# Kernel tuning notes

Hardware: AMD Instinct MI355X
Metric: run time of the kernel (lower is better)

Reference implementation:

```python
import jax, jax.numpy as jnp
import numpy as np

LN_EPS = 1e-5

def _layernorm(x, w, b):
    mu = jnp.mean(x, axis=-1, keepdims=True)
    var = jnp.mean(jnp.square(x - mu), axis=-1, keepdims=True)
    return (x - mu) * jax.lax.rsqrt(var + LN_EPS) * w + b

def setup_inputs() -> dict:
    key = jax.random.key(0)
    ks = jax.random.split(key, 8)
    B, T, D, E = 8, 4096, 1024, 4
    inner = 4 * D
    x = jax.random.normal(ks[0], (B, T, D), dtype=jnp.float32)
    router_prob = jax.random.uniform(ks[1], (B, T, E), dtype=jnp.float32)
    alpha = jnp.ones((), dtype=jnp.float32)
    norm_w = jnp.ones((D,), dtype=jnp.float32)
    norm_b = jnp.zeros((D,), dtype=jnp.float32)
    l1_w = jax.random.normal(ks[2], (inner, D), dtype=jnp.float32) * 0.02
    l1_b = jax.random.normal(ks[3], (inner,), dtype=jnp.float32) * 0.02
    l2_w = jax.random.normal(ks[4], (D, inner), dtype=jnp.float32) * 0.02
    l2_b = jax.random.normal(ks[5], (D,), dtype=jnp.float32) * 0.02
    return {"x": x, "router_prob": router_prob, "alpha": alpha,
            "norm_w": norm_w, "norm_b": norm_b,
            "l1_w": l1_w, "l1_b": l1_b, "l2_w": l2_w, "l2_b": l2_b}

def reference(x, router_prob, alpha, norm_w, norm_b, l1_w, l1_b, l2_w, l2_b):
    B, T, D = x.shape
    E = router_prob.shape[2]
    n = T // E  # tokens per expert (contiguous slices)
    outs = []
    for e in range(E):  # small fixed loop; each expert has a different width m
        xs = x[:, e * n:(e + 1) * n, :]              # [B,n,D]
        h = _layernorm(xs, norm_w, norm_b)
        m = D // (2 ** e)                             # Matryoshka width
        he = h[:, :, :m]                              # [B,n,m]
        # dropout is a no-op in eval mode
        inner = jax.nn.gelu(jnp.einsum('btm,im->bti', he, l1_w[:, :m]) + l1_b,
                            approximate=False)        # [B,n,4D]
        out = jnp.einsum('bti,mi->btm', inner, l2_w[:m, :]) + l2_b[:m]  # [B,n,m]
        out = jnp.pad(out, ((0, 0), (0, 0), (0, D - m)))
        scale = alpha * router_prob[:, e * n:(e + 1) * n, e] + 1.0      # [B,n]
        outs.append(xs + scale[:, :, None] * out)
    return jnp.concatenate(outs, axis=1)
```

## Files before the change

### kernel.cpp

```cpp
#include <hip/hip_runtime.h>
#include <cstdint>

#define DD     1024
#define NINNER 4096
#define NTOK   32768
#define MROWS  8192

typedef unsigned short u16;
typedef __bf16 bf16x8 __attribute__((ext_vector_type(8)));
typedef float  f32x4  __attribute__((ext_vector_type(4)));

__device__ __forceinline__ u16 f2bf(float f) {
    union { float f; uint32_t u; } a; a.f = f;
    uint32_t r = a.u + 0x7fffu + ((a.u >> 16) & 1u);
    return (u16)(r >> 16);
}

__device__ __forceinline__ void async16(const void* g, void* l) {
    __builtin_amdgcn_global_load_lds(
        (const __attribute__((address_space(1))) void*)g,
        (__attribute__((address_space(3))) void*)l,
        16, 0, 0);
}

__global__ __launch_bounds__(256) void cast_w(
    const float* __restrict__ w1, const float* __restrict__ w2,
    u16* __restrict__ w1b, u16* __restrict__ w2b)
{
    int idx = blockIdx.x * 256 + threadIdx.x;
    const int n1 = (NINNER * DD) / 4;
    float4 v; ushort4 o;
    if (idx < n1) {
        v = ((const float4*)w1)[idx];
        o.x = f2bf(v.x); o.y = f2bf(v.y); o.z = f2bf(v.z); o.w = f2bf(v.w);
        ((ushort4*)w1b)[idx] = o;
    } else {
        int j = idx - n1;
        v = ((const float4*)w2)[j];
        o.x = f2bf(v.x); o.y = f2bf(v.y); o.z = f2bf(v.z); o.w = f2bf(v.w);
        ((ushort4*)w2b)[j] = o;
    }
}

__global__ __launch_bounds__(256) void ln_kernel(
    const float* __restrict__ x, const float* __restrict__ nw,
    const float* __restrict__ nb, const float* __restrict__ l2b,
    const float* __restrict__ rp, const float* __restrict__ alphap,
    u16* __restrict__ h, float* __restrict__ out)
{
    const int row = blockIdx.x;
    const int tid = threadIdx.x;
    const float4 v = ((const float4*)(x + (size_t)row * DD))[tid];
    float s  = v.x + v.y + v.z + v.w;
    float s2 = v.x*v.x + v.y*v.y + v.z*v.z + v.w*v.w;
#pragma unroll
    for (int o = 32; o > 0; o >>= 1) {
        s  += __shfl_down(s,  o, 64);
        s2 += __shfl_down(s2, o, 64);
    }
    __shared__ float as1[4], as2[4];
    if ((tid & 63) == 0) { as1[tid >> 6] = s; as2[tid >> 6] = s2; }
    __syncthreads();
    const float S  = as1[0] + as1[1] + as1[2] + as1[3];
    const float S2 = as2[0] + as2[1] + as2[2] + as2[3];
    const float mu  = S  * (1.0f / 1024.0f);
    const float var = S2 * (1.0f / 1024.0f) - mu * mu;
    const float rs  = rsqrtf(var + 1e-5f);
    const float4 w4 = ((const float4*)nw)[tid];
    const float4 b4 = ((const float4*)nb)[tid];
    ushort4 hv;
    hv.x = f2bf((v.x - mu) * rs * w4.x + b4.x);
    hv.y = f2bf((v.y - mu) * rs * w4.y + b4.y);
    hv.z = f2bf((v.z - mu) * rs * w4.z + b4.z);
    hv.w = f2bf((v.w - mu) * rs * w4.w + b4.w);
    ((ushort4*)(h + (size_t)row * DD))[tid] = hv;

    const int e = (row >> 10) & 3;
    const int m = DD >> e;
    float4 o4;
    if (tid * 4 < m) {
        const float sc = alphap[0] * rp[(size_t)row * 4 + e] + 1.0f;
        const float4 lb = ((const float4*)l2b)[tid];
        o4.x = v.x + sc * lb.x; o4.y = v.y + sc * lb.y;
        o4.z = v.z + sc * lb.z; o4.w = v.w + sc * lb.w;
    } else {
        o4 = v;
    }
    ((float4*)(out + (size_t)row * DD))[tid] = o4;
}


__global__ __launch_bounds__(256) void gemm1(
    const u16* __restrict__ h, const u16* __restrict__ w1b,
    const float* __restrict__ l1b, u16* __restrict__ inner,
    int K, int e)
{
    __shared__ u16 lA[128 * 64];
    __shared__ u16 lB[128 * 64];
    const int tid  = threadIdx.x;
    const int lane = tid & 63;
    const int w    = tid >> 6;
    const int wr   = w >> 1, wc = w & 1;
    const int bm = blockIdx.y, bn = blockIdx.x;

    f32x4 acc[4][4] = {};

    const int srow = (lane >> 3);
    const int soff = ((lane & 7) ^ srow) * 8;

    for (int kt = 0; kt < K; kt += 64) {
#pragma unroll
        for (int i = 0; i < 4; ++i) {
            const int c   = w * 4 + i;
            const int row = c * 8 + srow;
            const int rl  = bm * 128 + row;
            const int g   = ((rl >> 10) << 12) + (e << 10) + (rl & 1023);
            async16(h + (size_t)g * DD + kt + soff, &lA[c * 512]);
        }
#pragma unroll
        for (int i = 0; i < 4; ++i) {
            const int c   = w * 4 + i;
            const int row = c * 8 + srow;
            async16(w1b + (size_t)(bn * 128 + row) * DD + kt + soff, &lB[c * 512]);
        }
        __syncthreads();
#pragma unroll
        for (int kk = 0; kk < 2; ++kk) {
            const int sg = ((kk * 4 + (lane >> 4)) ^ (lane & 7)) * 8;
            bf16x8 af[4], bq[4];
#pragma unroll
            for (int i = 0; i < 4; ++i)
                af[i] = *(const bf16x8*)&lA[(wr * 64 + i * 16 + (lane & 15)) * 64 + sg];
#pragma unroll
            for (int i = 0; i < 4; ++i)
                bq[i] = *(const bf16x8*)&lB[(wc * 64 + i * 16 + (lane & 15)) * 64 + sg];
#pragma unroll
            for (int mi = 0; mi < 4; ++mi)
#pragma unroll
                for (int ni = 0; ni < 4; ++ni)
                    acc[mi][ni] = __builtin_amdgcn_mfma_f32_16x16x32_bf16(
                        af[mi], bq[ni], acc[mi][ni], 0, 0, 0);
        }
        __syncthreads();
    }

    const int cbase = bn * 128 + wc * 64 + (lane & 15);
    const int rbase = bm * 128 + wr * 64 + (lane >> 4) * 4;
#pragma unroll
    for (int ni = 0; ni < 4; ++ni) {
        const int col = cbase + ni * 16;
        const float bias = l1b[col];
#pragma unroll
        for (int mi = 0; mi < 4; ++mi) {
            const int r0 = rbase + mi * 16;
#pragma unroll
            for (int r = 0; r < 4; ++r) {
                const float vv = acc[mi][ni][r] + bias;
                const float gg = 0.5f * vv * (1.0f + erff(vv * 0.7071067811865476f));
                inner[(size_t)(r0 + r) * NINNER + col] = f2bf(gg);
            }
        }
    }
}

__global__ __launch_bounds__(256) void gemm2(
    const u16* __restrict__ inner, const u16* __restrict__ w2b,
    const float* __restrict__ rp, const float* __restrict__ alphap,
    float* __restrict__ out, int e, int lgBn, int lgCPB)
{
    __shared__ u16 lA[128 * 64];
    __shared__ u16 lB[128 * 64];
    const int tid  = threadIdx.x;
    const int lane = tid & 63;
    const int w    = tid >> 6;
    const int wr   = w >> 1, wc = w & 1;

    const int id    = blockIdx.x;
    const int xcd   = id & 7;
    const int j     = id >> 3;
    const int bm    = ((j >> lgCPB) << 3) | xcd;
    const int chunk = j & ((1 << lgCPB) - 1);
    const int bn    = chunk & ((1 << lgBn) - 1);
    const int s     = chunk >> lgBn;
    const int Kc    = NINNER >> (lgCPB - lgBn);
    const int k0    = s * Kc;

    f32x4 acc[4][4] = {};
    const int srow = (lane >> 3);
    const int soff = ((lane & 7) ^ srow) * 8;

    for (int kt = k0; kt < k0 + Kc; kt += 64) {
#pragma unroll
        for (int i = 0; i < 4; ++i) {
            const int c   = w * 4 + i;
            const int row = c * 8 + srow;
            async16(inner + (size_t)(bm * 128 + row) * NINNER + kt + soff, &lA[c * 512]);
        }
#pragma unroll
        for (int i = 0; i < 4; ++i) {
            const int c   = w * 4 + i;
            const int row = c * 8 + srow;
            async16(w2b + (size_t)(bn * 128 + row) * NINNER + kt + soff, &lB[c * 512]);
        }
        __syncthreads();
#pragma unroll
        for (int kk = 0; kk < 2; ++kk) {
            const int sg = ((kk * 4 + (lane >> 4)) ^ (lane & 7)) * 8;
            bf16x8 af[4], bq[4];
#pragma unroll
            for (int i = 0; i < 4; ++i)
                af[i] = *(const bf16x8*)&lA[(wr * 64 + i * 16 + (lane & 15)) * 64 + sg];
#pragma unroll
            for (int i = 0; i < 4; ++i)
                bq[i] = *(const bf16x8*)&lB[(wc * 64 + i * 16 + (lane & 15)) * 64 + sg];
#pragma unroll
            for (int mi = 0; mi < 4; ++mi)
#pragma unroll
                for (int ni = 0; ni < 4; ++ni)
                    acc[mi][ni] = __builtin_amdgcn_mfma_f32_16x16x32_bf16(
                        af[mi], bq[ni], acc[mi][ni], 0, 0, 0);
        }
        __syncthreads();
    }

    const float alpha = alphap[0];
    const int cbase = bn * 128 + wc * 64 + (lane & 15);
    const int rbase = bm * 128 + wr * 64 + (lane >> 4) * 4;
#pragma unroll
    for (int mi = 0; mi < 4; ++mi) {
#pragma unroll
        for (int r = 0; r < 4; ++r) {
            const int rl = rbase + mi * 16 + r;
            const int g  = ((rl >> 10) << 12) + (e << 10) + (rl & 1023);
            const float sc = alpha * rp[(size_t)g * 4 + e] + 1.0f;
#pragma unroll
            for (int ni = 0; ni < 4; ++ni) {
                const int col = cbase + ni * 16;
                unsafeAtomicAdd(out + (size_t)g * DD + col, sc * acc[mi][ni][r]);
            }
        }
    }
}

extern "C" void kernel_launch(void* const* d_in, const int* in_sizes, int n_in,
                              void* d_out, int out_size, void* d_ws, size_t ws_size,
                              hipStream_t stream) {
    const float* x     = (const float*)d_in[0];
    const float* rp    = (const float*)d_in[1];
    const float* alpha = (const float*)d_in[2];
    const float* nw    = (const float*)d_in[3];
    const float* nb    = (const float*)d_in[4];
    const float* l1w   = (const float*)d_in[5];
    const float* l1b   = (const float*)d_in[6];
    const float* l2w   = (const float*)d_in[7];
    const float* l2b   = (const float*)d_in[8];
    float* out = (float*)d_out;

    char* ws = (char*)d_ws;
    if (ws_size < ((size_t)144 << 20)) return;
    u16* h     = (u16*)(ws);
    u16* inner = (u16*)(ws + ((size_t)64 << 20));
    u16* w1b   = (u16*)(ws + ((size_t)128 << 20));
    u16* w2b   = (u16*)(ws + ((size_t)136 << 20));

    cast_w<<<8192, 256, 0, stream>>>(l1w, l2w, w1b, w2b);
    ln_kernel<<<NTOK, 256, 0, stream>>>(x, nw, nb, l2b, rp, alpha, h, out);
    static const int lgBn_t[4]  = {3, 2, 1, 0};
    static const int lgCPB_t[4] = {4, 4, 4, 3};
    for (int e = 0; e < 4; ++e) {
        const int m = DD >> e;
        gemm1<<<dim3(NINNER / 128, MROWS / 128), 256, 0, stream>>>(h, w1b, l1b, inner, m, e);
        gemm2<<<64 << lgCPB_t[e], 256, 0, stream>>>(inner, w2b, rp, alpha, out, e,
                                                    lgBn_t[e], lgCPB_t[e]);
    }
}
```

Before: 837.6 us.

## Add 256x256-tile 8-wave GEMM kernels with phased prefetch for wide experts

Adds gemm1_big and gemm2_big, which use 256x256 output tiles with 512 threads and double-buffered LDS staged in halves. Each k-step is split into four MFMA phases, with barriers, raised wave priority and vmcnt waits interleaved so global-to-LDS loads overlap compute. The big kernels run for the wider experts (gemm1 for e<2, gemm2 for e<3) to get more data reuse per tile. The cost is far fewer blocks per launch, heavier register and LDS use per block, and hand-placed barriers that could stall the pipeline.

```diff
diff --git a/kernel.cpp b/kernel.cpp
--- a/kernel.cpp
+++ b/kernel.cpp
@@ -89,14 +89,13 @@
     ((float4*)(out + (size_t)row * DD))[tid] = o4;
 }
 
-
 __global__ __launch_bounds__(256) void gemm1(
     const u16* __restrict__ h, const u16* __restrict__ w1b,
     const float* __restrict__ l1b, u16* __restrict__ inner,
     int K, int e)
 {
-    __shared__ u16 lA[128 * 64];
-    __shared__ u16 lB[128 * 64];
+    __shared__ __align__(16) u16 lA[128 * 64];
+    __shared__ __align__(16) u16 lB[128 * 64];
     const int tid  = threadIdx.x;
     const int lane = tid & 63;
     const int w    = tid >> 6;
@@ -168,8 +167,8 @@
     const float* __restrict__ rp, const float* __restrict__ alphap,
     float* __restrict__ out, int e, int lgBn, int lgCPB)
 {
-    __shared__ u16 lA[128 * 64];
-    __shared__ u16 lB[128 * 64];
+    __shared__ __align__(16) u16 lA[128 * 64];
+    __shared__ __align__(16) u16 lB[128 * 64];
     const int tid  = threadIdx.x;
     const int lane = tid & 63;
     const int w    = tid >> 6;
@@ -237,6 +236,255 @@
             for (int ni = 0; ni < 4; ++ni) {
                 const int col = cbase + ni * 16;
                 unsafeAtomicAdd(out + (size_t)g * DD + col, sc * acc[mi][ni][r]);
+            }
+        }
+    }
+}
+
+
+#define PH_PRE()  do { asm volatile("" ::: "memory");                        \
+                       __builtin_amdgcn_s_barrier();                         \
+                       asm volatile("s_waitcnt lgkmcnt(0)" ::: "memory");    \
+                       __builtin_amdgcn_sched_barrier(0);                    \
+                       __builtin_amdgcn_s_setprio(1); } while (0)
+#define PH_POST(VM) do { __builtin_amdgcn_s_setprio(0);                      \
+                       if (VM) { asm volatile("s_waitcnt vmcnt(4)" ::: "memory"); } \
+                       else    { asm volatile("" ::: "memory"); }            \
+                       __builtin_amdgcn_s_barrier(); } while (0)
+
+__global__ __launch_bounds__(512, 2) void gemm1_big(
+    const u16* __restrict__ h, const u16* __restrict__ w1b,
+    const float* __restrict__ l1b, u16* __restrict__ inner,
+    int K, int e)
+{
+    __shared__ __align__(16) u16 lA[2][2][8192];
+    __shared__ __align__(16) u16 lB[2][2][8192];
+    const int tid  = threadIdx.x;
+    const int lane = tid & 63;
+    const int w    = tid >> 6;
+    const int qr   = w >> 2;
+    const int qc   = w & 3;
+    const int l15  = lane & 15, l4g = lane >> 4, l7 = lane & 7;
+    const int lrow = lane >> 3;
+    const int soff = ((lane & 7) ^ lrow) * 8;
+
+    const int id  = blockIdx.x;
+    const int swz = (id & 7) * 64 + (id >> 3);
+    const int bm  = swz >> 4, bn = swz & 15;
+
+    const int NT = K >> 6;
+
+    f32x4 acc[4][4][2] = {};
+    bf16x8 af[4][2], bq[2][2];
+
+    auto STAGE_A = [&](int buf, int half, int kt) {
+        const int rbase = bm * 256 + half * 128;
+#pragma unroll
+        for (int i = 0; i < 2; ++i) {
+            const int c  = i * 8 + w;
+            const int rl = rbase + c * 8 + lrow;
+            const int g  = ((rl >> 10) << 12) + (e << 10) + (rl & 1023);
+            async16(h + (size_t)g * DD + kt + soff, &lA[buf][half][c * 512]);
+        }
+    };
+    auto STAGE_B = [&](int buf, int half, int kt) {
+        const int rbase = bn * 256 + half * 128;
+#pragma unroll
+        for (int i = 0; i < 2; ++i) {
+            const int c   = i * 8 + w;
+            const int row = rbase + c * 8 + lrow;
+            async16(w1b + (size_t)row * DD + kt + soff, &lB[buf][half][c * 512]);
+        }
+    };
+    auto DSA = [&](int buf, int half) {
+#pragma unroll
+        for (int mi = 0; mi < 4; ++mi)
+#pragma unroll
+            for (int kk = 0; kk < 2; ++kk)
+                af[mi][kk] = *(const bf16x8*)&lA[buf][half]
+                    [(qr * 64 + mi * 16 + l15) * 64 + ((kk * 4 + l4g) ^ l7) * 8];
+    };
+    auto DSB = [&](int buf, int half) {
+#pragma unroll
+        for (int ni = 0; ni < 2; ++ni)
+#pragma unroll
+            for (int kk = 0; kk < 2; ++kk)
+                bq[ni][kk] = *(const bf16x8*)&lB[buf][half]
+                    [(qc * 32 + ni * 16 + l15) * 64 + ((kk * 4 + l4g) ^ l7) * 8];
+    };
+    auto MM = [&](f32x4 (&ac)[4][2]) {
+#pragma unroll
+        for (int mi = 0; mi < 4; ++mi)
+#pragma unroll
+            for (int ni = 0; ni < 2; ++ni) {
+                f32x4 c = ac[mi][ni];
+                c = __builtin_amdgcn_mfma_f32_16x16x32_bf16(af[mi][0], bq[ni][0], c, 0, 0, 0);
+                c = __builtin_amdgcn_mfma_f32_16x16x32_bf16(af[mi][1], bq[ni][1], c, 0, 0, 0);
+                ac[mi][ni] = c;
+            }
+    };
+
+    STAGE_A(0, 0, 0); STAGE_B(0, 0, 0); STAGE_B(0, 1, 0); STAGE_A(0, 1, 0);
+    asm volatile("s_waitcnt vmcnt(4)" ::: "memory");
+    __builtin_amdgcn_s_barrier();
+
+    for (int t = 0; t < NT; ++t) {
+        const int cur = t & 1, nxt = cur ^ 1;
+        const int kn  = (t + 1 < NT ? t + 1 : t) << 6;
+        DSA(cur, 0); DSB(cur, 0);
+        STAGE_A(nxt, 0, kn);
+        PH_PRE();  MM(acc[0]);  PH_POST(1);
+        DSB(cur, 1);
+        STAGE_B(nxt, 0, kn);
+        PH_PRE();  MM(acc[1]);  PH_POST(1);
+        DSA(cur, 1); DSB(cur, 0);
+        STAGE_B(nxt, 1, kn);
+        PH_PRE();  MM(acc[2]);  PH_POST(0);
+        DSB(cur, 1);
+        STAGE_A(nxt, 1, kn);
+        PH_PRE();  MM(acc[3]);  PH_POST(1);
+    }
+
+#pragma unroll
+    for (int nh = 0; nh < 2; ++nh) {
+#pragma unroll
+        for (int ni = 0; ni < 2; ++ni) {
+            const int col  = bn * 256 + nh * 128 + qc * 32 + ni * 16 + l15;
+            const float bias = l1b[col];
+#pragma unroll
+            for (int mh = 0; mh < 2; ++mh) {
+                const int rb = bm * 256 + mh * 128 + qr * 64 + l4g * 4;
+#pragma unroll
+                for (int mi = 0; mi < 4; ++mi) {
+#pragma unroll
+                    for (int r = 0; r < 4; ++r) {
+                        const float vv = acc[mh * 2 + nh][mi][ni][r] + bias;
+                        const float gg = 0.5f * vv * (1.0f + erff(vv * 0.7071067811865476f));
+                        inner[(size_t)(rb + mi * 16 + r) * NINNER + col] = f2bf(gg);
+                    }
+                }
+            }
+        }
+    }
+}
+
+__global__ __launch_bounds__(512, 2) void gemm2_big(
+    const u16* __restrict__ inner, const u16* __restrict__ w2b,
+    const float* __restrict__ rp, const float* __restrict__ alphap,
+    float* __restrict__ out, int e, int lgNBN)
+{
+    __shared__ __align__(16) u16 lA[2][2][8192];
+    __shared__ __align__(16) u16 lB[2][2][8192];
+    const int tid  = threadIdx.x;
+    const int lane = tid & 63;
+    const int w    = tid >> 6;
+    const int qr   = w >> 2;
+    const int qc   = w & 3;
+    const int l15  = lane & 15, l4g = lane >> 4, l7 = lane & 7;
+    const int lrow = lane >> 3;
+    const int soff = ((lane & 7) ^ lrow) * 8;
+
+    const int id    = blockIdx.x;
+    const int xcd   = id & 7;
+    const int j     = id >> 3;
+    const int bm    = ((j >> 3) << 3) | xcd;
+    const int chunk = j & 7;
+    const int bn    = chunk & ((1 << lgNBN) - 1);
+    const int s     = chunk >> lgNBN;
+    const int Kc    = NINNER >> (3 - lgNBN);
+    const int k0    = s * Kc;
+    const int NT    = Kc >> 6;
+
+    f32x4 acc[4][4][2] = {};
+    bf16x8 af[4][2], bq[2][2];
+
+    auto STAGE_A = [&](int buf, int half, int kt) {
+        const int rbase = bm * 256 + half * 128;
+#pragma unroll
+        for (int i = 0; i < 2; ++i) {
+            const int c   = i * 8 + w;
+            const int row = rbase + c * 8 + lrow;
+            async16(inner + (size_t)row * NINNER + kt + soff, &lA[buf][half][c * 512]);
+        }
+    };
+    auto STAGE_B = [&](int buf, int half, int kt) {
+        const int rbase = bn * 256 + half * 128;
+#pragma unroll
+        for (int i = 0; i < 2; ++i) {
+            const int c   = i * 8 + w;
+            const int row = rbase + c * 8 + lrow;
+            async16(w2b + (size_t)row * NINNER + kt + soff, &lB[buf][half][c * 512]);
+        }
+    };
+    auto DSA = [&](int buf, int half) {
+#pragma unroll
+        for (int mi = 0; mi < 4; ++mi)
+#pragma unroll
+            for (int kk = 0; kk < 2; ++kk)
+                af[mi][kk] = *(const bf16x8*)&lA[buf][half]
+                    [(qr * 64 + mi * 16 + l15) * 64 + ((kk * 4 + l4g) ^ l7) * 8];
+    };
+    auto DSB = [&](int buf, int half) {
+#pragma unroll
+        for (int ni = 0; ni < 2; ++ni)
+#pragma unroll
+            for (int kk = 0; kk < 2; ++kk)
+                bq[ni][kk] = *(const bf16x8*)&lB[buf][half]
+                    [(qc * 32 + ni * 16 + l15) * 64 + ((kk * 4 + l4g) ^ l7) * 8];
+    };
+    auto MM = [&](f32x4 (&ac)[4][2]) {
+#pragma unroll
+        for (int mi = 0; mi < 4; ++mi)
+#pragma unroll
+            for (int ni = 0; ni < 2; ++ni) {
+                f32x4 c = ac[mi][ni];
+                c = __builtin_amdgcn_mfma_f32_16x16x32_bf16(af[mi][0], bq[ni][0], c, 0, 0, 0);
+                c = __builtin_amdgcn_mfma_f32_16x16x32_bf16(af[mi][1], bq[ni][1], c, 0, 0, 0);
+                ac[mi][ni] = c;
+            }
+    };
+
+    STAGE_A(0, 0, k0); STAGE_B(0, 0, k0); STAGE_B(0, 1, k0); STAGE_A(0, 1, k0);
+    asm volatile("s_waitcnt vmcnt(4)" ::: "memory");
+    __builtin_amdgcn_s_barrier();
+
+    for (int t = 0; t < NT; ++t) {
+        const int cur = t & 1, nxt = cur ^ 1;
+        const int kn  = k0 + ((t + 1 < NT ? t + 1 : t) << 6);
+        DSA(cur, 0); DSB(cur, 0);
+        STAGE_A(nxt, 0, kn);
+        PH_PRE();  MM(acc[0]);  PH_POST(1);
+        DSB(cur, 1);
+        STAGE_B(nxt, 0, kn);
+        PH_PRE();  MM(acc[1]);  PH_POST(1);
+        DSA(cur, 1); DSB(cur, 0);
+        STAGE_B(nxt, 1, kn);
+        PH_PRE();  MM(acc[2]);  PH_POST(0);
+        DSB(cur, 1);
+        STAGE_A(nxt, 1, kn);
+        PH_PRE();  MM(acc[3]);  PH_POST(1);
+    }
+
+    const float alpha = alphap[0];
+#pragma unroll
+    for (int mh = 0; mh < 2; ++mh) {
+        const int rb = bm * 256 + mh * 128 + qr * 64 + l4g * 4;
+#pragma unroll
+        for (int mi = 0; mi < 4; ++mi) {
+#pragma unroll
+            for (int r = 0; r < 4; ++r) {
+                const int rl = rb + mi * 16 + r;
+                const int g  = ((rl >> 10) << 12) + (e << 10) + (rl & 1023);
+                const float sc = alpha * rp[(size_t)g * 4 + e] + 1.0f;
+#pragma unroll
+                for (int nh = 0; nh < 2; ++nh) {
+#pragma unroll
+                    for (int ni = 0; ni < 2; ++ni) {
+                        const int col = bn * 256 + nh * 128 + qc * 32 + ni * 16 + l15;
+                        unsafeAtomicAdd(out + (size_t)g * DD + col,
+                                        sc * acc[mh * 2 + nh][mi][ni][r]);
+                    }
+                }
             }
         }
     }
@@ -265,12 +513,15 @@
 
     cast_w<<<8192, 256, 0, stream>>>(l1w, l2w, w1b, w2b);
     ln_kernel<<<NTOK, 256, 0, stream>>>(x, nw, nb, l2b, rp, alpha, h, out);
-    static const int lgBn_t[4]  = {3, 2, 1, 0};
-    static const int lgCPB_t[4] = {4, 4, 4, 3};
     for (int e = 0; e < 4; ++e) {
         const int m = DD >> e;
-        gemm1<<<dim3(NINNER / 128, MROWS / 128), 256, 0, stream>>>(h, w1b, l1b, inner, m, e);
-        gemm2<<<64 << lgCPB_t[e], 256, 0, stream>>>(inner, w2b, rp, alpha, out, e,
-                                                    lgBn_t[e], lgCPB_t[e]);
-    }
-}
+        if (e < 2)
+            gemm1_big<<<512, 512, 0, stream>>>(h, w1b, l1b, inner, m, e);
+        else
+            gemm1<<<dim3(NINNER / 128, MROWS / 128), 256, 0, stream>>>(h, w1b, l1b, inner, m, e);
+        if (e < 3)
+            gemm2_big<<<256, 512, 0, stream>>>(inner, w2b, rp, alpha, out, e, 2 - e);
+        else
+            gemm2<<<64 << 3, 256, 0, stream>>>(inner, w2b, rp, alpha, out, e, 0, 3);
+    }
+}
```

Result: slower. 872.5 us (+4.2%).

## Add pipelined 256x256 gemm1 and non-split-K multi-buffered gemm2 kernels

Applied to the files above, without the earlier changes.

Adds a 512-thread gemm1_big kernel with 256x256 tiles, a double-buffered LDS pipeline with partial vmcnt waits and setprio around the MFMA blocks. It is used for the two widest experts. gemm2 is replaced by a templated gemm2_nk that does not split K. It uses 2 or 3 LDS buffers and per-expert tile heights, and replaces atomic adds with plain read-modify-write stores. This removes the split-K atomic traffic and overlaps global loads with compute, but each block now runs a longer serial K loop and fewer blocks are launched for the narrow experts.

```diff
diff --git a/kernel.cpp b/kernel.cpp
--- a/kernel.cpp
+++ b/kernel.cpp
@@ -22,6 +22,10 @@
         (__attribute__((address_space(3))) void*)l,
         16, 0, 0);
 }
+
+#define BARRIER() do { asm volatile("" ::: "memory");              \
+                       __builtin_amdgcn_s_barrier();               \
+                       asm volatile("" ::: "memory"); } while (0)
 
 __global__ __launch_bounds__(256) void cast_w(
     const float* __restrict__ w1, const float* __restrict__ w2,
@@ -89,14 +93,13 @@
     ((float4*)(out + (size_t)row * DD))[tid] = o4;
 }
 
-
 __global__ __launch_bounds__(256) void gemm1(
     const u16* __restrict__ h, const u16* __restrict__ w1b,
     const float* __restrict__ l1b, u16* __restrict__ inner,
     int K, int e)
 {
-    __shared__ u16 lA[128 * 64];
-    __shared__ u16 lB[128 * 64];
+    __shared__ __align__(16) u16 lA[128 * 64];
+    __shared__ __align__(16) u16 lB[128 * 64];
     const int tid  = threadIdx.x;
     const int lane = tid & 63;
     const int w    = tid >> 6;
@@ -163,80 +166,244 @@
     }
 }
 
-__global__ __launch_bounds__(256) void gemm2(
+__global__ __launch_bounds__(512, 2) void gemm1_big(
+    const u16* __restrict__ h, const u16* __restrict__ w1b,
+    const float* __restrict__ l1b, u16* __restrict__ inner,
+    int K, int e)
+{
+    __shared__ __align__(16) u16 lA[2][2][8192];
+    __shared__ __align__(16) u16 lB[2][2][8192];
+    const int tid  = threadIdx.x;
+    const int lane = tid & 63;
+    const int w    = tid >> 6;
+    const int qr   = w >> 2;
+    const int qc   = w & 3;
+    const int l15  = lane & 15, l4g = lane >> 4, l7 = lane & 7;
+    const int lrow = lane >> 3;
+    const int soff = (l7 ^ lrow) * 8;
+
+    const int id  = blockIdx.x;
+    const int swz = (id & 7) * 64 + (id >> 3);
+    const int bm  = swz >> 4, bn = swz & 15;
+
+    const int NT = K >> 6;
+
+    size_t aOff[2][2], bOff[2][2];
+#pragma unroll
+    for (int hf = 0; hf < 2; ++hf)
+#pragma unroll
+        for (int i = 0; i < 2; ++i) {
+            const int c  = i * 8 + w;
+            const int rl = bm * 256 + hf * 128 + c * 8 + lrow;
+            const int g  = ((rl >> 10) << 12) + (e << 10) + (rl & 1023);
+            aOff[hf][i]  = (size_t)g * DD + soff;
+            const int rb = bn * 256 + hf * 128 + c * 8 + lrow;
+            bOff[hf][i]  = (size_t)rb * DD + soff;
+        }
+
+    f32x4 acc[4][4][2] = {};
+    bf16x8 af[4][2], bq[2][2];
+
+    auto STAGE_ALL = [&](int buf, int kt) {
+        async16(h   + aOff[0][0] + kt, &lA[buf][0][w * 512]);
+        async16(h   + aOff[0][1] + kt, &lA[buf][0][(8 + w) * 512]);
+        async16(w1b + bOff[0][0] + kt, &lB[buf][0][w * 512]);
+        async16(w1b + bOff[0][1] + kt, &lB[buf][0][(8 + w) * 512]);
+        async16(w1b + bOff[1][0] + kt, &lB[buf][1][w * 512]);
+        async16(w1b + bOff[1][1] + kt, &lB[buf][1][(8 + w) * 512]);
+        async16(h   + aOff[1][0] + kt, &lA[buf][1][w * 512]);
+        async16(h   + aOff[1][1] + kt, &lA[buf][1][(8 + w) * 512]);
+    };
+    auto DSA = [&](int buf, int half) {
+#pragma unroll
+        for (int mi = 0; mi < 4; ++mi)
+#pragma unroll
+            for (int kk = 0; kk < 2; ++kk)
+                af[mi][kk] = *(const bf16x8*)&lA[buf][half]
+                    [(qr * 64 + mi * 16 + l15) * 64 + ((kk * 4 + l4g) ^ l7) * 8];
+    };
+    auto DSB = [&](int buf, int half) {
+#pragma unroll
+        for (int ni = 0; ni < 2; ++ni)
+#pragma unroll
+            for (int kk = 0; kk < 2; ++kk)
+                bq[ni][kk] = *(const bf16x8*)&lB[buf][half]
+                    [(qc * 32 + ni * 16 + l15) * 64 + ((kk * 4 + l4g) ^ l7) * 8];
+    };
+    auto MM = [&](f32x4 (&ac)[4][2]) {
+#pragma unroll
+        for (int mi = 0; mi < 4; ++mi)
+#pragma unroll
+            for (int ni = 0; ni < 2; ++ni) {
+                f32x4 c = ac[mi][ni];
+                c = __builtin_amdgcn_mfma_f32_16x16x32_bf16(af[mi][0], bq[ni][0], c, 0, 0, 0);
+                c = __builtin_amdgcn_mfma_f32_16x16x32_bf16(af[mi][1], bq[ni][1], c, 0, 0, 0);
+                ac[mi][ni] = c;
+            }
+    };
+
+    STAGE_ALL(0, 0);
+    asm volatile("s_waitcnt vmcnt(4)" ::: "memory");
+    BARRIER();
+
+    for (int t = 0; t < NT; ++t) {
+        const int cur = t & 1, nxt = cur ^ 1;
+        const int kn  = (t + 1 < NT ? t + 1 : t) << 6;
+        STAGE_ALL(nxt, kn);
+        DSA(cur, 0);
+        DSB(cur, 0);
+        __builtin_amdgcn_s_setprio(1);
+        MM(acc[0]);
+        __builtin_amdgcn_s_setprio(0);
+        asm volatile("s_waitcnt vmcnt(10)" ::: "memory");
+        BARRIER();
+        DSB(cur, 1);
+        __builtin_amdgcn_s_setprio(1);
+        MM(acc[1]);
+        __builtin_amdgcn_s_setprio(0);
+        asm volatile("s_waitcnt vmcnt(8)" ::: "memory");
+        BARRIER();
+        DSA(cur, 1);
+        DSB(cur, 0);
+        __builtin_amdgcn_s_setprio(1);
+        MM(acc[2]);
+        __builtin_amdgcn_s_setprio(0);
+        DSB(cur, 1);
+        __builtin_amdgcn_s_setprio(1);
+        MM(acc[3]);
+        __builtin_amdgcn_s_setprio(0);
+        asm volatile("s_waitcnt vmcnt(4)" ::: "memory");
+        BARRIER();
+    }
+
+#pragma unroll
+    for (int nh = 0; nh < 2; ++nh) {
+#pragma unroll
+        for (int ni = 0; ni < 2; ++ni) {
+            const int col  = bn * 256 + nh * 128 + qc * 32 + ni * 16 + l15;
+            const float bias = l1b[col];
+#pragma unroll
+            for (int mh = 0; mh < 2; ++mh) {
+                const int rb = bm * 256 + mh * 128 + qr * 64 + l4g * 4;
+#pragma unroll
+                for (int mi = 0; mi < 4; ++mi) {
+#pragma unroll
+                    for (int r = 0; r < 4; ++r) {
+                        const float vv = acc[mh * 2 + nh][mi][ni][r] + bias;
+                        const float gg = 0.5f * vv * (1.0f + erff(vv * 0.7071067811865476f));
+                        inner[(size_t)(rb + mi * 16 + r) * NINNER + col] = f2bf(gg);
+                    }
+                }
+            }
+        }
+    }
+}
+
+template<int BM, int NBUF>
+__global__ __launch_bounds__(BM * 2, 2) void gemm2_nk(
     const u16* __restrict__ inner, const u16* __restrict__ w2b,
     const float* __restrict__ rp, const float* __restrict__ alphap,
-    float* __restrict__ out, int e, int lgBn, int lgCPB)
+    float* __restrict__ out, int e, int lgBn)
 {
-    __shared__ u16 lA[128 * 64];
-    __shared__ u16 lB[128 * 64];
+    constexpr int WAVES = BM / 32;
+    constexpr int LB    = 512 / BM;
+    constexpr int NT    = NINNER / 64;
+
+    __shared__ __align__(16) u16 lA[NBUF][BM * 64];
+    __shared__ __align__(16) u16 lB[NBUF][128 * 64];
+
     const int tid  = threadIdx.x;
     const int lane = tid & 63;
     const int w    = tid >> 6;
     const int wr   = w >> 1, wc = w & 1;
-
-    const int id    = blockIdx.x;
-    const int xcd   = id & 7;
-    const int j     = id >> 3;
-    const int bm    = ((j >> lgCPB) << 3) | xcd;
-    const int chunk = j & ((1 << lgCPB) - 1);
-    const int bn    = chunk & ((1 << lgBn) - 1);
-    const int s     = chunk >> lgBn;
-    const int Kc    = NINNER >> (lgCPB - lgBn);
-    const int k0    = s * Kc;
+    const int l15  = lane & 15, l4g = lane >> 4, l7 = lane & 7;
+    const int lrow = lane >> 3;
+    const int soff = (l7 ^ lrow) * 8;
+
+    const int id  = blockIdx.x;
+    const int xcd = id & 7, j = id >> 3;
+    const int bm  = ((j >> lgBn) << 3) | xcd;
+    const int bn  = j & ((1 << lgBn) - 1);
+
+    size_t aOff[4], bOff[LB];
+#pragma unroll
+    for (int i = 0; i < 4; ++i) {
+        const int row = bm * BM + (i * WAVES + w) * 8 + lrow;
+        aOff[i] = (size_t)row * NINNER + soff;
+    }
+#pragma unroll
+    for (int i = 0; i < LB; ++i) {
+        const int row = bn * 128 + (i * WAVES + w) * 8 + lrow;
+        bOff[i] = (size_t)row * NINNER + soff;
+    }
+
+    auto STAGE = [&](int buf, int kt) {
+#pragma unroll
+        for (int i = 0; i < 4; ++i)
+            async16(inner + aOff[i] + kt, &lA[buf][(i * WAVES + w) * 512]);
+#pragma unroll
+        for (int i = 0; i < LB; ++i)
+            async16(w2b + bOff[i] + kt, &lB[buf][(i * WAVES + w) * 512]);
+    };
 
     f32x4 acc[4][4] = {};
-    const int srow = (lane >> 3);
-    const int soff = ((lane & 7) ^ srow) * 8;
-
-    for (int kt = k0; kt < k0 + Kc; kt += 64) {
-#pragma unroll
-        for (int i = 0; i < 4; ++i) {
-            const int c   = w * 4 + i;
-            const int row = c * 8 + srow;
-            async16(inner + (size_t)(bm * 128 + row) * NINNER + kt + soff, &lA[c * 512]);
-        }
-#pragma unroll
-        for (int i = 0; i < 4; ++i) {
-            const int c   = w * 4 + i;
-            const int row = c * 8 + srow;
-            async16(w2b + (size_t)(bn * 128 + row) * NINNER + kt + soff, &lB[c * 512]);
-        }
-        __syncthreads();
-#pragma unroll
-        for (int kk = 0; kk < 2; ++kk) {
-            const int sg = ((kk * 4 + (lane >> 4)) ^ (lane & 7)) * 8;
-            bf16x8 af[4], bq[4];
-#pragma unroll
-            for (int i = 0; i < 4; ++i)
-                af[i] = *(const bf16x8*)&lA[(wr * 64 + i * 16 + (lane & 15)) * 64 + sg];
-#pragma unroll
-            for (int i = 0; i < 4; ++i)
-                bq[i] = *(const bf16x8*)&lB[(wc * 64 + i * 16 + (lane & 15)) * 64 + sg];
-#pragma unroll
-            for (int mi = 0; mi < 4; ++mi)
-#pragma unroll
-                for (int ni = 0; ni < 4; ++ni)
-                    acc[mi][ni] = __builtin_amdgcn_mfma_f32_16x16x32_bf16(
-                        af[mi], bq[ni], acc[mi][ni], 0, 0, 0);
-        }
-        __syncthreads();
+    bf16x8 af[4][2], bq[4][2];
+
+    STAGE(0, 0);
+    if constexpr (NBUF == 3) STAGE(1, 64);
+    if constexpr (BM == 256)      asm volatile("s_waitcnt vmcnt(6)"  ::: "memory");
+    else if constexpr (BM == 64)  asm volatile("s_waitcnt vmcnt(12)" ::: "memory");
+    else                          asm volatile("s_waitcnt vmcnt(0)"  ::: "memory");
+    BARRIER();
+
+    int cur = 0, stg = NBUF - 1;
+    for (int t = 0; t < NT; ++t) {
+        const int ts = (t + NBUF - 1 < NT ? t + NBUF - 1 : NT - 1);
+        STAGE(stg, ts * 64);
+#pragma unroll
+        for (int mi = 0; mi < 4; ++mi)
+#pragma unroll
+            for (int kk = 0; kk < 2; ++kk)
+                af[mi][kk] = *(const bf16x8*)&lA[cur]
+                    [(wr * 64 + mi * 16 + l15) * 64 + ((kk * 4 + l4g) ^ l7) * 8];
+#pragma unroll
+        for (int ni = 0; ni < 4; ++ni)
+#pragma unroll
+            for (int kk = 0; kk < 2; ++kk)
+                bq[ni][kk] = *(const bf16x8*)&lB[cur]
+                    [(wc * 64 + ni * 16 + l15) * 64 + ((kk * 4 + l4g) ^ l7) * 8];
+        __builtin_amdgcn_s_setprio(1);
+#pragma unroll
+        for (int mi = 0; mi < 4; ++mi)
+#pragma unroll
+            for (int ni = 0; ni < 4; ++ni) {
+                f32x4 c = acc[mi][ni];
+                c = __builtin_amdgcn_mfma_f32_16x16x32_bf16(af[mi][0], bq[ni][0], c, 0, 0, 0);
+                c = __builtin_amdgcn_mfma_f32_16x16x32_bf16(af[mi][1], bq[ni][1], c, 0, 0, 0);
+                acc[mi][ni] = c;
+            }
+        __builtin_amdgcn_s_setprio(0);
+        if constexpr (BM == 256)      asm volatile("s_waitcnt vmcnt(6)"  ::: "memory");
+        else if constexpr (BM == 64)  asm volatile("s_waitcnt vmcnt(12)" ::: "memory");
+        else                          asm volatile("s_waitcnt vmcnt(0)"  ::: "memory");
+        BARRIER();
+        cur = (cur + 1 == NBUF) ? 0 : cur + 1;
+        stg = (stg + 1 == NBUF) ? 0 : stg + 1;
     }
 
     const float alpha = alphap[0];
-    const int cbase = bn * 128 + wc * 64 + (lane & 15);
-    const int rbase = bm * 128 + wr * 64 + (lane >> 4) * 4;
 #pragma unroll
     for (int mi = 0; mi < 4; ++mi) {
 #pragma unroll
         for (int r = 0; r < 4; ++r) {
-            const int rl = rbase + mi * 16 + r;
+            const int rl = bm * BM + wr * 64 + mi * 16 + l4g * 4 + r;
             const int g  = ((rl >> 10) << 12) + (e << 10) + (rl & 1023);
             const float sc = alpha * rp[(size_t)g * 4 + e] + 1.0f;
+            float* po = out + (size_t)g * DD;
 #pragma unroll
             for (int ni = 0; ni < 4; ++ni) {
-                const int col = cbase + ni * 16;
-                unsafeAtomicAdd(out + (size_t)g * DD + col, sc * acc[mi][ni][r]);
+                const int col = bn * 128 + wc * 64 + ni * 16 + l15;
+                po[col] += sc * acc[mi][ni][r];
             }
         }
     }
@@ -265,12 +432,17 @@
 
     cast_w<<<8192, 256, 0, stream>>>(l1w, l2w, w1b, w2b);
     ln_kernel<<<NTOK, 256, 0, stream>>>(x, nw, nb, l2b, rp, alpha, h, out);
-    static const int lgBn_t[4]  = {3, 2, 1, 0};
-    static const int lgCPB_t[4] = {4, 4, 4, 3};
     for (int e = 0; e < 4; ++e) {
         const int m = DD >> e;
-        gemm1<<<dim3(NINNER / 128, MROWS / 128), 256, 0, stream>>>(h, w1b, l1b, inner, m, e);
-        gemm2<<<64 << lgCPB_t[e], 256, 0, stream>>>(inner, w2b, rp, alpha, out, e,
-                                                    lgBn_t[e], lgCPB_t[e]);
-    }
-}
+        if (e < 2)
+            gemm1_big<<<512, 512, 0, stream>>>(h, w1b, l1b, inner, m, e);
+        else
+            gemm1<<<dim3(NINNER / 128, MROWS / 128), 256, 0, stream>>>(h, w1b, l1b, inner, m, e);
+        switch (e) {
+            case 0: gemm2_nk<256, 3><<<256, 512, 0, stream>>>(inner, w2b, rp, alpha, out, e, 3); break;
+            case 1: gemm2_nk<128, 2><<<256, 256, 0, stream>>>(inner, w2b, rp, alpha, out, e, 2); break;
+            case 2: gemm2_nk< 64, 3><<<256, 128, 0, stream>>>(inner, w2b, rp, alpha, out, e, 1); break;
+            case 3: gemm2_nk< 64, 3><<<128, 128, 0, stream>>>(inner, w2b, rp, alpha, out, e, 0); break;
+        }
+    }
+}
```

Result: slower. 893.2 us (+6.6%).
